# Performance work log

Hardware: AMD Instinct MI355X
Metric: run time of the kernel (lower is better)

The kernel has to match this reference:

```python
import jax, jax.numpy as jnp
import numpy as np

N = 50000      # nodes
DEG = 16       # fixed out-degree per row
E = N * DEG    # edges (CSR nnz)
H = 128        # hidden_size
NH = 8         # num_heads


def setup_inputs() -> dict:
    key = jax.random.key(0)
    ks = jax.random.split(key, 8)
    s = 1.0 / np.sqrt(H)
    h = jax.random.normal(ks[0], (N, H), jnp.float32)
    Wq = jax.random.normal(ks[1], (H, H), jnp.float32) * s
    bq = jax.random.normal(ks[2], (H,), jnp.float32) * 0.02
    Wk = jax.random.normal(ks[3], (H, H), jnp.float32) * s
    bk = jax.random.normal(ks[4], (H,), jnp.float32) * 0.02
    Wv = jax.random.normal(ks[5], (H, H), jnp.float32) * s
    bv = jax.random.normal(ks[6], (H,), jnp.float32) * 0.02
    row_ptr = jnp.arange(N + 1, dtype=jnp.int32) * DEG            # fixed-degree CSR
    col_ind = jax.random.randint(ks[7], (E,), 0, N, dtype=jnp.int32)
    return {"h": h, "Wq": Wq, "bq": bq, "Wk": Wk, "bk": bk, "Wv": Wv, "bv": bv,
            "row_ptr": row_ptr, "col_ind": col_ind, "num_heads": NH}


def reference(h, Wq, bq, Wk, bk, Wv, bv, row_ptr, col_ind, num_heads):
    n = h.shape[0]
    hidden = h.shape[1]
    head_dim = hidden // num_heads
    scaling = head_dim ** (-0.5)
    e = col_ind.shape[0]
    # CSR nnz -> row index per edge
    row = (jnp.searchsorted(row_ptr, jnp.arange(e, dtype=row_ptr.dtype), side="right") - 1).astype(jnp.int32)

    # projections; reshape to (N, head_dim, num_heads) exactly as in the torch code
    q = ((h @ Wq.T + bq) * scaling).reshape(n, head_dim, num_heads)
    k = (h @ Wk.T + bk).reshape(n, head_dim, num_heads)
    v = (h @ Wv.T + bv).reshape(n, head_dim, num_heads)

    # bsddmm: per-edge, per-head dot product over head_dim
    scores = jnp.einsum("edh,edh->eh", q[row], k[col_ind])      # [E, NH]

    # sparse row-wise softmax (segment softmax over edges of each row)
    m = jax.ops.segment_max(scores, row, num_segments=n)        # [N, NH]
    ex = jnp.exp(scores - m[row])
    denom = jax.ops.segment_sum(ex, row, num_segments=n)        # [N, NH]
    attn = ex / denom[row]                                      # [E, NH]

    # bspmm: out[i] = sum_{j in nbr(i)} attn[ij] * v[j]
    out = jax.ops.segment_sum(attn[:, None, :] * v[col_ind], row, num_segments=n)  # [N, head_dim, NH]
    return out.reshape(n, -1)
```

## Files before the change

kernel.cpp:

```cpp
#include <hip/hip_runtime.h>
#include <hip/hip_bf16.h>


typedef unsigned short ushort_t;
typedef unsigned int uint32;
typedef short short8 __attribute__((ext_vector_type(8)));
typedef short short4v __attribute__((ext_vector_type(4)));
typedef float f32x4 __attribute__((ext_vector_type(4)));

#define HID 128
#define DEG 16
#define OSTRIDE_LDS 132

__device__ __forceinline__ float bf2f(ushort_t u) {
  uint32 x = ((uint32)u) << 16;
  return __builtin_bit_cast(float, x);
}
__device__ __forceinline__ ushort_t f2bf(float f) {
  uint32 u = __builtin_bit_cast(uint32, f);
  u += 0x7fffu + ((u >> 16) & 1u);
  return (ushort_t)(u >> 16);
}

__device__ __forceinline__ void split2(float x, float y, uint32& hi, uint32& lo) {
  __hip_bfloat162 h2 = __float22bfloat162_rn(float2{x, y});
  __builtin_memcpy(&hi, &h2, 4);
  float hx = __builtin_bit_cast(float, hi << 16);
  float hy = __builtin_bit_cast(float, hi & 0xffff0000u);
  __hip_bfloat162 l2 = __float22bfloat162_rn(float2{x - hx, y - hy});
  __builtin_memcpy(&lo, &l2, 4);
}

__device__ __forceinline__ void split8v(float4 a, float4 b, short8& hi, short8& lo) {
  uint32* hu = (uint32*)&hi;
  uint32* lu = (uint32*)&lo;
  split2(a.x, a.y, hu[0], lu[0]);
  split2(a.z, a.w, hu[1], lu[1]);
  split2(b.x, b.y, hu[2], lu[2]);
  split2(b.z, b.w, hu[3], lu[3]);
}

__device__ __forceinline__ void split8p(const float* __restrict__ p, short8& hi, short8& lo) {
  float4 a = *(const float4*)p;
  float4 b = *(const float4*)(p + 4);
  split8v(a, b, hi, lo);
}

__global__ __launch_bounds__(256) void prep_kernel(
    const float* __restrict__ Wq, const float* __restrict__ Wk,
    const float* __restrict__ Wv,
    ushort_t* __restrict__ whi, ushort_t* __restrict__ wlo) {
  const int idx8 = (blockIdx.x * 256 + threadIdx.x) * 8;
  const float* W = (idx8 < 16384) ? Wq : (idx8 < 32768) ? Wk : Wv;
  const int off = idx8 & 16383;
  short8 hi, lo;
  split8p(W + off, hi, lo);
  *(short8*)(whi + idx8) = hi;
  *(short8*)(wlo + idx8) = lo;
}

__global__ __launch_bounds__(256) void qkv_fused_kernel(
    const float* __restrict__ h,
    const float* __restrict__ bq, const float* __restrict__ bk,
    const float* __restrict__ bv,
    const ushort_t* __restrict__ whi, const ushort_t* __restrict__ wlo,
    ushort_t* __restrict__ qs, ushort_t* __restrict__ ks, ushort_t* __restrict__ vs,
    int n) {
  __shared__ __align__(16) char lds_raw[65536];
  char* buf0 = lds_raw;
  char* buf1 = lds_raw + 32768;

  const int wave = threadIdx.x >> 6;
  const int l = threadIdx.x & 63;
  const int lm = l & 15;
  const int lq = l >> 4;
  const int m0 = blockIdx.x * 128 + wave * 32;

  int ar0 = m0 + lm;        if (ar0 >= n) ar0 = n - 1;
  int ar1 = m0 + 16 + lm;   if (ar1 >= n) ar1 = n - 1;
  const float* ap0 = h + (size_t)ar0 * HID + lq * 8;
  const float* ap1 = h + (size_t)ar1 * HID + lq * 8;
  short8 ah0[4], al0[4], ah1[4], al1[4];
#pragma unroll
  for (int kt = 0; kt < 4; kt++) {
    split8p(ap0 + kt * 32, ah0[kt], al0[kt]);
    split8p(ap1 + kt * 32, ah1[kt], al1[kt]);
  }

#pragma unroll 1
  for (int p = 0; p < 3; p++) {
    const ushort_t* __restrict__ Wh = whi + p * 16384;
    const ushort_t* __restrict__ Wl = wlo + p * 16384;
    const float* __restrict__ bias = (p == 0) ? bq : (p == 1) ? bk : bv;
    ushort_t* __restrict__ outp = (p == 0) ? qs : (p == 1) ? ks : vs;
    const int ostride = (p == 0) ? 256 : 128;
    const float scale = (p == 0) ? 0.25f : 1.0f;

#pragma unroll
    for (int jj = 0; jj < 8; jj++) {
      const int j = wave * 8 + jj, t = j >> 2, kt = j & 3;
      const int goff = (t * 16 + lm) * HID + kt * 32 + lq * 8;
      __builtin_amdgcn_global_load_lds(
          (const __attribute__((address_space(1))) void*)(Wh + goff),
          (__attribute__((address_space(3))) void*)(buf0 + j * 1024 + l * 16),
          16, 0, 0);
      __builtin_amdgcn_global_load_lds(
          (const __attribute__((address_space(1))) void*)(Wl + goff),
          (__attribute__((address_space(3))) void*)(buf1 + j * 1024 + l * 16),
          16, 0, 0);
    }
    __syncthreads();

    f32x4 acc[2][8];
#pragma unroll
    for (int f = 0; f < 2; f++)
#pragma unroll
      for (int t = 0; t < 8; t++) acc[f][t] = (f32x4){0.f, 0.f, 0.f, 0.f};

#pragma unroll
    for (int kt = 0; kt < 4; kt++) {
#pragma unroll
      for (int t = 0; t < 8; t++) {
        const int so = (t * 4 + kt) * 1024 + l * 16;
        short8 bh = *(const short8*)(buf0 + so);
        short8 bl = *(const short8*)(buf1 + so);
        acc[0][t] = __builtin_amdgcn_mfma_f32_16x16x32_bf16(ah0[kt], bh, acc[0][t], 0, 0, 0);
        acc[0][t] = __builtin_amdgcn_mfma_f32_16x16x32_bf16(al0[kt], bh, acc[0][t], 0, 0, 0);
        acc[0][t] = __builtin_amdgcn_mfma_f32_16x16x32_bf16(ah0[kt], bl, acc[0][t], 0, 0, 0);
        acc[1][t] = __builtin_amdgcn_mfma_f32_16x16x32_bf16(ah1[kt], bh, acc[1][t], 0, 0, 0);
        acc[1][t] = __builtin_amdgcn_mfma_f32_16x16x32_bf16(al1[kt], bh, acc[1][t], 0, 0, 0);
        acc[1][t] = __builtin_amdgcn_mfma_f32_16x16x32_bf16(ah1[kt], bl, acc[1][t], 0, 0, 0);
      }
    }
    __syncthreads();

    ushort_t* lo_ = (ushort_t*)lds_raw + wave * 32 * OSTRIDE_LDS;
#pragma unroll
    for (int t = 0; t < 8; t++) {
      const int col = t * 16 + lm;
      const float bv_ = bias[col];
#pragma unroll
      for (int f = 0; f < 2; f++) {
#pragma unroll
        for (int r = 0; r < 4; r++) {
          lo_[(f * 16 + lq * 4 + r) * OSTRIDE_LDS + col] = f2bf((acc[f][t][r] + bv_) * scale);
        }
      }
    }
    asm volatile("s_waitcnt lgkmcnt(0)" ::: "memory");
    __builtin_amdgcn_wave_barrier();

    const int rr = l >> 5;
    const int ch = l & 31;
#pragma unroll
    for (int it = 0; it < 16; it++) {
      const int rw = it * 2 + rr;
      const int grow = m0 + rw;
      short4v val = *(short4v*)(lo_ + rw * OSTRIDE_LDS + ch * 4);
      if (grow < n) *(short4v*)(outp + (size_t)grow * ostride + ch * 4) = val;
    }
    __syncthreads();
  }
}

__global__ __launch_bounds__(256) void attn_kernel(
    const int* __restrict__ col_ind,
    const ushort_t* __restrict__ qs, const ushort_t* __restrict__ ks,
    const ushort_t* __restrict__ vs, float* __restrict__ out, int n) {
  __shared__ __align__(16) float lds_attn[4 * DEG * 8];

  const int wv = threadIdx.x >> 6;
  const int l = threadIdx.x & 63;
  const int lm = l & 15;
  const int lq = l >> 4;

  int row = blockIdx.x * 4 + wv;
  if (row >= n) row = n - 1;
  const int eb = row * DEG;

  const int cm = col_ind[eb + lm];
  const ushort_t* kp = ks + (size_t)cm * HID + lq * 8;
  const ushort_t* qp = qs + (size_t)row * 256;

  short8 af[4];
  ushort_t qv[4];
#pragma unroll
  for (int kt = 0; kt < 4; kt++) {
    af[kt] = *(const short8*)(kp + kt * 32);
    qv[kt] = (lm < 8) ? qp[kt * 32 + lq * 8 + lm] : (ushort_t)0;
  }

  uint32 vreg[DEG];
#pragma unroll
  for (int e = 0; e < DEG; e++) {
    const int c = col_ind[eb + e];
    vreg[e] = *(const uint32*)(vs + (size_t)c * HID + 2 * l);
  }

  f32x4 acc = (f32x4){0.f, 0.f, 0.f, 0.f};
#pragma unroll
  for (int kt = 0; kt < 4; kt++) {
    short8 bf;
#pragma unroll
    for (int j = 0; j < 8; j++) bf[j] = (lm == j) ? (short)qv[kt] : (short)0;
    acc = __builtin_amdgcn_mfma_f32_16x16x32_bf16(af[kt], bf, acc, 0, 0, 0);
  }

  float m = fmaxf(fmaxf(acc[0], acc[1]), fmaxf(acc[2], acc[3]));
  m = fmaxf(m, __shfl_xor(m, 16, 64));
  m = fmaxf(m, __shfl_xor(m, 32, 64));
  float e0 = __expf(acc[0] - m), e1 = __expf(acc[1] - m);
  float e2 = __expf(acc[2] - m), e3 = __expf(acc[3] - m);
  float s = e0 + e1 + e2 + e3;
  s += __shfl_xor(s, 16, 64);
  s += __shfl_xor(s, 32, 64);
  const float inv = 1.0f / s;

  float* ap = &lds_attn[wv * (DEG * 8)];
  if (lm < 8) {
    ap[(lq * 4 + 0) * 8 + lm] = e0 * inv;
    ap[(lq * 4 + 1) * 8 + lm] = e1 * inv;
    ap[(lq * 4 + 2) * 8 + lm] = e2 * inv;
    ap[(lq * 4 + 3) * 8 + lm] = e3 * inv;
  }
  asm volatile("s_waitcnt lgkmcnt(0)" ::: "memory");
  __builtin_amdgcn_wave_barrier();

  const int h0 = 2 * (l & 3);
  float o0 = 0.f, o1 = 0.f;
#pragma unroll
  for (int e = 0; e < DEG; e++) {
    const float2 at = *(const float2*)(ap + e * 8 + h0);
    o0 += at.x * bf2f((ushort_t)(vreg[e] & 0xffffu));
    o1 += at.y * bf2f((ushort_t)(vreg[e] >> 16));
  }

  float2 o = {o0, o1};
  *(float2*)(out + (size_t)row * HID + 2 * l) = o;
}

extern "C" void kernel_launch(void* const* d_in, const int* in_sizes, int n_in,
                              void* d_out, int out_size, void* d_ws, size_t ws_size,
                              hipStream_t stream) {
  const float* h  = (const float*)d_in[0];
  const float* Wq = (const float*)d_in[1];
  const float* bq = (const float*)d_in[2];
  const float* Wk = (const float*)d_in[3];
  const float* bk = (const float*)d_in[4];
  const float* Wv = (const float*)d_in[5];
  const float* bv = (const float*)d_in[6];
  const int* col_ind = (const int*)d_in[8];

  const int n = in_sizes[0] / HID;

  ushort_t* ks  = (ushort_t*)d_ws;
  ushort_t* vs  = ks + (size_t)n * HID;
  ushort_t* whi = vs + (size_t)n * HID;
  ushort_t* wlo = whi + 3 * 16384;
  ushort_t* qs  = (ushort_t*)d_out;
  float* outf   = (float*)d_out;

  prep_kernel<<<24, 256, 0, stream>>>(Wq, Wk, Wv, whi, wlo);
  qkv_fused_kernel<<<(n + 127) / 128, 256, 0, stream>>>(h, bq, bk, bv, whi, wlo, qs, ks, vs, n);
  attn_kernel<<<(n + 3) / 4, 256, 0, stream>>>(col_ind, qs, ks, vs, outf, n);
}
```

Before: 173.3 us.

## Switch Q/K/V to head-major layout and process attention per head with transpose

```diff
diff --git a/kernel.cpp b/kernel.cpp
--- a/kernel.cpp
+++ b/kernel.cpp
@@ -64,7 +64,7 @@
     const float* __restrict__ bq, const float* __restrict__ bk,
     const float* __restrict__ bv,
     const ushort_t* __restrict__ whi, const ushort_t* __restrict__ wlo,
-    ushort_t* __restrict__ qs, ushort_t* __restrict__ ks, ushort_t* __restrict__ vs,
+    ushort_t* __restrict__ qh, ushort_t* __restrict__ kh, ushort_t* __restrict__ vh,
     int n) {
   __shared__ __align__(16) char lds_raw[65536];
   char* buf0 = lds_raw;
@@ -92,8 +92,7 @@
     const ushort_t* __restrict__ Wh = whi + p * 16384;
     const ushort_t* __restrict__ Wl = wlo + p * 16384;
     const float* __restrict__ bias = (p == 0) ? bq : (p == 1) ? bk : bv;
-    ushort_t* __restrict__ outp = (p == 0) ? qs : (p == 1) ? ks : vs;
-    const int ostride = (p == 0) ? 256 : 128;
+    ushort_t* __restrict__ outp = (p == 0) ? qh : (p == 1) ? kh : vh;
     const float scale = (p == 0) ? 0.25f : 1.0f;
 
 #pragma unroll
@@ -139,11 +138,12 @@
     for (int t = 0; t < 8; t++) {
       const int col = t * 16 + lm;
       const float bv_ = bias[col];
+      const int pos = (lm & 7) * 16 + 2 * t + (lm >> 3);
 #pragma unroll
       for (int f = 0; f < 2; f++) {
 #pragma unroll
         for (int r = 0; r < 4; r++) {
-          lo_[(f * 16 + lq * 4 + r) * OSTRIDE_LDS + col] = f2bf((acc[f][t][r] + bv_) * scale);
+          lo_[(f * 16 + lq * 4 + r) * OSTRIDE_LDS + pos] = f2bf((acc[f][t][r] + bv_) * scale);
         }
       }
     }
@@ -151,92 +151,112 @@
     __builtin_amdgcn_wave_barrier();
 
     const int rr = l >> 5;
-    const int ch = l & 31;
+    const int q = l & 31;
+    const int hh = q >> 2, part = q & 3;
 #pragma unroll
     for (int it = 0; it < 16; it++) {
       const int rw = it * 2 + rr;
       const int grow = m0 + rw;
-      short4v val = *(short4v*)(lo_ + rw * OSTRIDE_LDS + ch * 4);
-      if (grow < n) *(short4v*)(outp + (size_t)grow * ostride + ch * 4) = val;
+      short4v val = *(short4v*)(lo_ + rw * OSTRIDE_LDS + q * 4);
+      if (grow < n)
+        *(short4v*)(outp + ((size_t)hh * n + grow) * 16 + part * 4) = val;
     }
     __syncthreads();
   }
 }
 
-__global__ __launch_bounds__(256) void attn_kernel(
+__global__ __launch_bounds__(256) void attn_head_kernel(
     const int* __restrict__ col_ind,
-    const ushort_t* __restrict__ qs, const ushort_t* __restrict__ ks,
-    const ushort_t* __restrict__ vs, float* __restrict__ out, int n) {
-  __shared__ __align__(16) float lds_attn[4 * DEG * 8];
-
+    const ushort_t* __restrict__ qh, const ushort_t* __restrict__ kh,
+    const ushort_t* __restrict__ vh, float* __restrict__ oh, int n) {
+  const int head = blockIdx.x & 7;
+  const int tile = blockIdx.x >> 3;
   const int wv = threadIdx.x >> 6;
   const int l = threadIdx.x & 63;
-  const int lm = l & 15;
-  const int lq = l >> 4;
-
-  int row = blockIdx.x * 4 + wv;
-  if (row >= n) row = n - 1;
-  const int eb = row * DEG;
-
-  const int cm = col_ind[eb + lm];
-  const ushort_t* kp = ks + (size_t)cm * HID + lq * 8;
-  const ushort_t* qp = qs + (size_t)row * 256;
-
-  short8 af[4];
-  ushort_t qv[4];
-#pragma unroll
-  for (int kt = 0; kt < 4; kt++) {
-    af[kt] = *(const short8*)(kp + kt * 32);
-    qv[kt] = (lm < 8) ? qp[kt * 32 + lq * 8 + lm] : (ushort_t)0;
-  }
-
-  uint32 vreg[DEG];
-#pragma unroll
-  for (int e = 0; e < DEG; e++) {
-    const int c = col_ind[eb + e];
-    vreg[e] = *(const uint32*)(vs + (size_t)c * HID + 2 * l);
-  }
-
-  f32x4 acc = (f32x4){0.f, 0.f, 0.f, 0.f};
-#pragma unroll
-  for (int kt = 0; kt < 4; kt++) {
-    short8 bf;
-#pragma unroll
-    for (int j = 0; j < 8; j++) bf[j] = (lm == j) ? (short)qv[kt] : (short)0;
-    acc = __builtin_amdgcn_mfma_f32_16x16x32_bf16(af[kt], bf, acc, 0, 0, 0);
-  }
-
-  float m = fmaxf(fmaxf(acc[0], acc[1]), fmaxf(acc[2], acc[3]));
-  m = fmaxf(m, __shfl_xor(m, 16, 64));
-  m = fmaxf(m, __shfl_xor(m, 32, 64));
-  float e0 = __expf(acc[0] - m), e1 = __expf(acc[1] - m);
-  float e2 = __expf(acc[2] - m), e3 = __expf(acc[3] - m);
-  float s = e0 + e1 + e2 + e3;
-  s += __shfl_xor(s, 16, 64);
-  s += __shfl_xor(s, 32, 64);
-  const float inv = 1.0f / s;
-
-  float* ap = &lds_attn[wv * (DEG * 8)];
-  if (lm < 8) {
-    ap[(lq * 4 + 0) * 8 + lm] = e0 * inv;
-    ap[(lq * 4 + 1) * 8 + lm] = e1 * inv;
-    ap[(lq * 4 + 2) * 8 + lm] = e2 * inv;
-    ap[(lq * 4 + 3) * 8 + lm] = e3 * inv;
-  }
-  asm volatile("s_waitcnt lgkmcnt(0)" ::: "memory");
-  __builtin_amdgcn_wave_barrier();
-
-  const int h0 = 2 * (l & 3);
-  float o0 = 0.f, o1 = 0.f;
-#pragma unroll
-  for (int e = 0; e < DEG; e++) {
-    const float2 at = *(const float2*)(ap + e * 8 + h0);
-    o0 += at.x * bf2f((ushort_t)(vreg[e] & 0xffffu));
-    o1 += at.y * bf2f((ushort_t)(vreg[e] >> 16));
-  }
-
-  float2 o = {o0, o1};
-  *(float2*)(out + (size_t)row * HID + 2 * l) = o;
+  const int e = l & 15;
+  const int g = l >> 4;
+
+  const ushort_t* kb = kh + (size_t)head * n * 16;
+  const ushort_t* vb = vh + (size_t)head * n * 16;
+  const ushort_t* qb = qh + (size_t)head * n * 16;
+  float* ob = oh + (size_t)head * n * 16;
+
+  const int row0 = tile * 64 + wv * 16;
+#pragma unroll 4
+  for (int it = 0; it < 16; it++) {
+    int row = row0 + it;
+    if (row >= n) row = n - 1;
+    const int c = col_ind[row * DEG + e];
+    short4v k4 = *(const short4v*)(kb + (size_t)c * 16 + g * 4);
+    short4v v4 = *(const short4v*)(vb + (size_t)c * 16 + g * 4);
+    short4v q4 = *(const short4v*)(qb + (size_t)row * 16 + g * 4);
+
+    float s = bf2f((ushort_t)k4[0]) * bf2f((ushort_t)q4[0]);
+    s = fmaf(bf2f((ushort_t)k4[1]), bf2f((ushort_t)q4[1]), s);
+    s = fmaf(bf2f((ushort_t)k4[2]), bf2f((ushort_t)q4[2]), s);
+    s = fmaf(bf2f((ushort_t)k4[3]), bf2f((ushort_t)q4[3]), s);
+    s += __shfl_xor(s, 16, 64);
+    s += __shfl_xor(s, 32, 64);
+
+    float m = s;
+    m = fmaxf(m, __shfl_xor(m, 1, 64));
+    m = fmaxf(m, __shfl_xor(m, 2, 64));
+    m = fmaxf(m, __shfl_xor(m, 4, 64));
+    m = fmaxf(m, __shfl_xor(m, 8, 64));
+    float ex = __expf(s - m);
+    float sum = ex;
+    sum += __shfl_xor(sum, 1, 64);
+    sum += __shfl_xor(sum, 2, 64);
+    sum += __shfl_xor(sum, 4, 64);
+    sum += __shfl_xor(sum, 8, 64);
+    const float a = ex / sum;
+
+    float o0 = a * bf2f((ushort_t)v4[0]);
+    float o1 = a * bf2f((ushort_t)v4[1]);
+    float o2 = a * bf2f((ushort_t)v4[2]);
+    float o3 = a * bf2f((ushort_t)v4[3]);
+#pragma unroll
+    for (int d = 1; d <= 8; d <<= 1) {
+      o0 += __shfl_xor(o0, d, 64);
+      o1 += __shfl_xor(o1, d, 64);
+      o2 += __shfl_xor(o2, d, 64);
+      o3 += __shfl_xor(o3, d, 64);
+    }
+    if (e == 0) {
+      float4 o = {o0, o1, o2, o3};
+      *(float4*)(ob + (size_t)row * 16 + g * 4) = o;
+    }
+  }
+}
+
+__global__ __launch_bounds__(256) void transpose_kernel(
+    const float* __restrict__ oh, float* __restrict__ out, int n) {
+  __shared__ float lds_t[64 * 132];
+  const int t = threadIdx.x;
+  const int r0 = blockIdx.x * 64;
+
+#pragma unroll
+  for (int hh = 0; hh < 8; hh++) {
+    int row = r0 + (t >> 2);
+    if (row >= n) row = n - 1;
+    float4 v = *(const float4*)(oh + ((size_t)hh * n + row) * 16 + (t & 3) * 4);
+    *(float4*)(&lds_t[(t >> 2) * 132 + hh * 16 + (t & 3) * 4]) = v;
+  }
+  __syncthreads();
+
+#pragma unroll
+  for (int rnd = 0; rnd < 8; rnd++) {
+    const int rloc = rnd * 8 + (t >> 5);
+    const int row = r0 + rloc;
+    const int j0 = (t & 31) * 4;
+    const float* lr = &lds_t[rloc * 132];
+    float4 o;
+    o.x = lr[((j0 + 0) & 7) * 16 + ((j0 + 0) >> 3)];
+    o.y = lr[((j0 + 1) & 7) * 16 + ((j0 + 1) >> 3)];
+    o.z = lr[((j0 + 2) & 7) * 16 + ((j0 + 2) >> 3)];
+    o.w = lr[((j0 + 3) & 7) * 16 + ((j0 + 3) >> 3)];
+    if (row < n) *(float4*)(out + (size_t)row * HID + j0) = o;
+  }
 }
 
 extern "C" void kernel_launch(void* const* d_in, const int* in_sizes, int n_in,
@@ -253,14 +273,17 @@
 
   const int n = in_sizes[0] / HID;
 
-  ushort_t* ks  = (ushort_t*)d_ws;
-  ushort_t* vs  = ks + (size_t)n * HID;
-  ushort_t* whi = vs + (size_t)n * HID;
+  ushort_t* kh  = (ushort_t*)d_ws;
+  ushort_t* vh  = kh + (size_t)n * HID;
+  ushort_t* whi = vh + (size_t)n * HID;
   ushort_t* wlo = whi + 3 * 16384;
-  ushort_t* qs  = (ushort_t*)d_out;
+  ushort_t* qh  = (ushort_t*)d_out;
+  float* oh     = (float*)d_in[0];
   float* outf   = (float*)d_out;
 
+  const int tiles = (n + 63) / 64;
   prep_kernel<<<24, 256, 0, stream>>>(Wq, Wk, Wv, whi, wlo);
-  qkv_fused_kernel<<<(n + 127) / 128, 256, 0, stream>>>(h, bq, bk, bv, whi, wlo, qs, ks, vs, n);
-  attn_kernel<<<(n + 3) / 4, 256, 0, stream>>>(col_ind, qs, ks, vs, outf, n);
-}
+  qkv_fused_kernel<<<(n + 127) / 128, 256, 0, stream>>>(h, bq, bk, bv, whi, wlo, qh, kh, vh, n);
+  attn_head_kernel<<<8 * tiles, 256, 0, stream>>>(col_ind, qh, kh, vh, oh, n);
+  transpose_kernel<<<tiles, 256, 0, stream>>>(oh, outf, n);
+}
```

Result: slower. 245.5 us (+41.7%).
